# Kernel tuning notes

Measured on AMD Instinct MI355X. Metric: run time of the kernel, lower is better.

The kernel has to match this reference:

```python
import jax, jax.numpy as jnp
import numpy as np
from jax import lax

HEADS = 8
DIM_HEAD = 64
MODALITIES = 8
QUERY_DIM = 128
INNER = HEADS * DIM_HEAD  # 512


def _conv(x, w):
    # x: (b, Cin, H, W), w: (Cout, Cin, kh, kw), VALID padding (padding done manually)
    return lax.conv_general_dilated(x, w, window_strides=(1, 1), padding='VALID',
                                    dimension_numbers=('NCHW', 'OIHW', 'NCHW'))


def _reflect_pad_w(x):
    # ReflectionPad2d((2,2,0,0)): pad width (last) axis by 2 on each side
    return jnp.pad(x, ((0, 0), (0, 0), (0, 0), (2, 2)), mode='reflect')


def setup_inputs() -> dict:
    key = jax.random.key(0)
    k1, k2, k3, k4 = jax.random.split(key, 4)
    b, n, m, c = 2, 4096, MODALITIES, QUERY_DIM
    x = jax.random.normal(k1, (b, n, m, c), dtype=jnp.float32)
    Wq = jax.random.normal(k2, (INNER, c, 1, 5), dtype=jnp.float32) * 0.02
    Wkv = jax.random.normal(k3, (2 * INNER, c, 1, 5), dtype=jnp.float32) * 0.02
    Wout = jax.random.normal(k4, (c * m, INNER, m, 5), dtype=jnp.float32) * 0.02
    return {"x": x, "Wq": Wq, "Wkv": Wkv, "Wout": Wout}


def reference(x, Wq, Wkv, Wout):
    b, n, m, c = x.shape
    h, d = HEADS, DIM_HEAD
    scale = d ** -0.5

    xp = _reflect_pad_w(jnp.transpose(x, (0, 3, 2, 1)))  # (b, c, m, n+4)
    q = _conv(xp, Wq)                                     # (b, h*d, m, n)
    kv = _conv(xp, Wkv)                                   # (b, 2*h*d, m, n)
    k, v = kv[:, :h * d], kv[:, h * d:]

    # channel axis (h d) split: h outer, d inner -> (b, h, d, m, n)
    q = q.reshape(b, h, d, m, n)
    k = k.reshape(b, h, d, m, n)
    v = v.reshape(b, h, d, m, n)

    # attention over sequence axis n; feature dim is (m d) per head
    sim = jnp.einsum('bhdmi,bhdmj->bhij', q, k) * scale   # (b, h, n, n)
    attn = jax.nn.softmax(sim, axis=-1)
    out = jnp.einsum('bhij,bhdmj->bhdmi', attn, v)        # (b, h, d, m, n)

    out = out.reshape(b, h * d, m, n)                     # 'b (h d) m n'
    o = _conv(_reflect_pad_w(out), Wout)                  # (b, c*m, 1, n)
    o = o.reshape(b, c, m, 1, n)[:, :, :, 0, :]           # squeeze height-1 dim -> (b, c, m, n)
    return o.reshape(x.shape)                             # torch .view(x_shape) is a raw reshape
```

## Files before the change

### kernel.cpp

```cpp
#include <hip/hip_runtime.h>
#include <stdint.h>


typedef __attribute__((ext_vector_type(8))) short short8;
typedef __attribute__((ext_vector_type(4))) short short4v;
typedef __attribute__((ext_vector_type(2))) short short2v;
typedef __attribute__((ext_vector_type(4))) float f32x4;
typedef __attribute__((ext_vector_type(16))) float f32x16;

__device__ __forceinline__ f32x4 mfma16(short8 a, short8 b, f32x4 c) {
  return __builtin_amdgcn_mfma_f32_16x16x32_bf16(a, b, c, 0, 0, 0);
}
__device__ __forceinline__ f32x16 mfma32(short8 a, short8 b, f32x16 c) {
  return __builtin_amdgcn_mfma_f32_32x32x16_bf16(a, b, c, 0, 0, 0);
}

__device__ __forceinline__ unsigned short f2bf(float f) {
  union { float f; uint32_t u; } v; v.f = f;
  uint32_t r = (v.u + 0x7fffu + ((v.u >> 16) & 1u)) >> 16;
  return (unsigned short)r;
}

__device__ __forceinline__ uint32_t cvtpk(float lo, float hi) {
  uint32_t r;
  asm volatile("v_cvt_pk_bf16_f32 %0, %1, %2" : "=v"(r) : "v"(lo), "v"(hi));
  return r;
}
__device__ __forceinline__ void plswap(uint32_t& a, uint32_t& b) {
  asm volatile("v_permlane32_swap_b32 %0, %1" : "+v"(a), "+v"(b));
}

__device__ __forceinline__ int refl4096(int p) {
  p = p < 0 ? -p : p;
  return p >= 4096 ? 8190 - p : p;
}

__device__ __forceinline__ void gl_lds16(const void* g, void* l) {
  __builtin_amdgcn_global_load_lds(
      (const __attribute__((address_space(1))) void*)g,
      (__attribute__((address_space(3))) void*)l, 16, 0, 0);
}

__global__ void k_convw_qkv(const float* __restrict__ Wq,
                            const float* __restrict__ Wkv,
                            unsigned short* __restrict__ out) {
  int e = blockIdx.x * 256 + threadIdx.x;
  int oc = e / 640, k = e - oc * 640;
  int ci = k & 127, t = k >> 7;
  float w = (oc < 512) ? Wq[oc * 640 + ci * 5 + t]
                       : Wkv[(oc - 512) * 640 + ci * 5 + t];
  out[e] = f2bf(w);
}

__global__ __launch_bounds__(256)
void k_convw_out(const float* __restrict__ Wout,
                 unsigned short* __restrict__ out) {
  __shared__ unsigned short row_l[20480];
  const int oc = blockIdx.x;
  const int tid = threadIdx.x;
  const float* src = Wout + (size_t)oc * 20480;
#pragma unroll
  for (int i0 = 0; i0 < 5120; i0 += 256) {
    int i = i0 + tid;
    f32x4 v = *(const f32x4*)(src + (size_t)i * 4);
    short4v pk;
    pk[0] = (short)f2bf(v[0]); pk[1] = (short)f2bf(v[1]);
    pk[2] = (short)f2bf(v[2]); pk[3] = (short)f2bf(v[3]);
    *(short4v*)(row_l + i * 4) = pk;
  }
  __syncthreads();
  unsigned short* drow = out + (size_t)oc * 20480;
#pragma unroll
  for (int r0 = 0; r0 < 20480; r0 += 512) {
    int e = r0 + tid * 2;
    int t0 = e >> 12, ft0 = e & 4095;
    int t1 = (e + 1) >> 12, ft1 = (e + 1) & 4095;
    short2v pk;
    pk[0] = (short)row_l[(ft0 >> 3) * 40 + (ft0 & 7) * 5 + t0];
    pk[1] = (short)row_l[(ft1 >> 3) * 40 + (ft1 & 7) * 5 + t1];
    *(short2v*)(drow + e) = pk;
  }
}

__global__ __launch_bounds__(256, 2)
void k_qkv(const float* __restrict__ x, const unsigned short* __restrict__ Wb,
           unsigned short* __restrict__ Qg, unsigned short* __restrict__ Kg,
           unsigned short* __restrict__ Vg, int b) {
  __shared__ __align__(16) unsigned short As[128 * 64];
  __shared__ __align__(16) unsigned short Bs[128 * 64];
  const int tid = threadIdx.x;
  const int lane = tid & 63, w = tid >> 6;
  const int wr = w >> 1, wc = w & 1;
  const int l15 = lane & 15, lg = lane >> 4;
  const int p0 = blockIdx.x * 128;
  const int ocb = blockIdx.y * 128;
  const int m = blockIdx.z;

  f32x4 acc[4][4];
#pragma unroll
  for (int i = 0; i < 4; i++)
#pragma unroll
    for (int j = 0; j < 4; j++) acc[i][j] = (f32x4){0.f, 0.f, 0.f, 0.f};

  for (int ks = 0; ks < 10; ks++) {
    const int t = ks >> 1;
    const int ci0 = (ks & 1) << 6;
    __syncthreads();
#pragma unroll
    for (int rr = 0; rr < 8; rr++) {
      int slot = tid + (rr << 8);
      int row = slot >> 4, c4 = slot & 15;
      int xn = refl4096(p0 + row - 2 + t);
      const f32x4 v = *(const f32x4*)(x + ((size_t)b * 4096 + xn) * 1024 +
                                      m * 128 + ci0 + (c4 << 2));
      short4v pk;
      pk[0] = (short)f2bf(v[0]); pk[1] = (short)f2bf(v[1]);
      pk[2] = (short)f2bf(v[2]); pk[3] = (short)f2bf(v[3]);
      int byte = (row << 7) + ((((c4 >> 1) ^ (row & 7))) << 4) + ((c4 & 1) << 3);
      *(short4v*)((char*)As + byte) = pk;
    }
#pragma unroll
    for (int c = 0; c < 4; c++) {
      int sb = ((c << 2) + w) << 6;
      int slot = sb + lane;
      int row = slot >> 3, cc = slot & 7;
      int cs = cc ^ (row & 7);
      gl_lds16(Wb + (size_t)(ocb + row) * 640 + (ks << 6) + (cs << 3),
               (char*)Bs + (size_t)sb * 16);
    }
    __syncthreads();
#pragma unroll
    for (int kk = 0; kk < 2; kk++) {
      short8 af[4], bq[4];
#pragma unroll
      for (int i = 0; i < 4; i++) {
        int row = (wr << 6) + (i << 4) + l15;
        af[i] = *(const short8*)((char*)As + (row << 7) +
                                 ((((kk << 2) + lg) ^ (row & 7)) << 4));
      }
#pragma unroll
      for (int j = 0; j < 4; j++) {
        int row = (wc << 6) + (j << 4) + l15;
        bq[j] = *(const short8*)((char*)Bs + (row << 7) +
                                 ((((kk << 2) + lg) ^ (row & 7)) << 4));
      }
#pragma unroll
      for (int i = 0; i < 4; i++)
#pragma unroll
        for (int j = 0; j < 4; j++) acc[i][j] = mfma16(af[i], bq[j], acc[i][j]);
    }
  }

  const int region = ocb >> 9;
  const float QSCALE = 0.18033688f;
#pragma unroll
  for (int i = 0; i < 4; i++) {
    const int posb = p0 + (wr << 6) + (i << 4) + (lg << 2);
#pragma unroll
    for (int j = 0; j < 4; j++) {
      const int oc = ocb + (wc << 6) + (j << 4) + l15;
      const int ocr = oc & 511;
      const int hh = ocr >> 6, dd = ocr & 63;
      const int f = (dd << 3) + m;
      if (region == 0) {
        size_t base = (size_t)hh * 4096 * 512 + f;
#pragma unroll
        for (int r = 0; r < 4; r++)
          Qg[base + (size_t)(posb + r) * 512] = f2bf(acc[i][j][r] * QSCALE);
      } else if (region == 1) {
        size_t base = (size_t)hh * 4096 * 512 + f;
#pragma unroll
        for (int r = 0; r < 4; r++)
          Kg[base + (size_t)(posb + r) * 512] = f2bf(acc[i][j][r]);
      } else {
        short4v pk;
#pragma unroll
        for (int r = 0; r < 4; r++) pk[r] = (short)f2bf(acc[i][j][r]);
        *(short4v*)(Vg + ((size_t)hh * 512 + f) * 4096 + posb) = pk;
      }
    }
  }
}

__global__ __launch_bounds__(512, 2)
void k_attn(const unsigned short* __restrict__ Qg,
            const unsigned short* __restrict__ Kg,
            const unsigned short* __restrict__ Vg,
            unsigned short* __restrict__ AO) {
  __shared__ __align__(16) char lds[139776];
  char* Kt = lds;
  char* Vt0 = lds + 32768;
  char* Vt1 = lds + 65536;
  char* Sx = lds + 98304;
  float* Ls = (float*)(lds + 139264);

  const int tid = threadIdx.x;
  const int lane = tid & 63, w = tid >> 6;
  const int l31 = lane & 31, hi = lane >> 5;
  const int wpair = w >> 1, whalf = w & 1;
  const int h = blockIdx.y;
  const int qbase = blockIdx.x * 128 + wpair * 32;
  const int fh = whalf << 8;

  const size_t kb = (size_t)h * 4096 * 512;
  const size_t vb = (size_t)h * 512 * 4096;

  short8 q[16];
  {
    const unsigned short* qp =
        Qg + ((size_t)h * 4096 + qbase + l31) * 512 + fh + hi * 8;
#pragma unroll
    for (int ks = 0; ks < 16; ks++) q[ks] = *(const short8*)(qp + ks * 16);
  }

  f32x16 o[8];
#pragma unroll
  for (int t = 0; t < 8; t++)
#pragma unroll
    for (int e = 0; e < 16; e++) o[t][e] = 0.f;
  float lacc = 0.f;

  const int rb = l31 >> 1;
  const int swz = rb & 7;
  const int cg0 = ((l31 & 1) << 2) + hi;
  const int voff1 = rb * 128 + ((cg0 ^ swz) << 4);
  const int voff2 = rb * 128 + (((cg0 + 2) ^ swz) << 4);

  char* sxw = Sx + w * 5120 + lane * 80;
  char* sxp = Sx + (w ^ 1) * 5120 + lane * 80;

  union U { uint32_t d[4]; short8 s; };

  auto stageK = [&](int it) {
    const int key0 = it << 5;
#pragma unroll
    for (int i = 0; i < 4; i++) {
      int s = tid + (i << 9);
      int r = s >> 6, c = s & 63;
      gl_lds16(Kg + kb + (size_t)(key0 + r) * 512 + ((c ^ r) << 3),
               Kt + (size_t)s * 16);
    }
  };
  auto stageV = [&](int it, char* Vt) {
    const int key0 = it << 5;
#pragma unroll
    for (int i = 0; i < 4; i++) {
      int s = tid + (i << 9);
      int rp = s >> 3, c = s & 7;
      int cu = c ^ (rp & 7);
      int f = (rp << 1) + (cu >> 2);
      gl_lds16(Vg + vb + (size_t)f * 4096 + key0 + ((cu & 3) << 3),
               Vt + (size_t)s * 16);
    }
  };

  stageK(0);
  stageV(0, Vt0);

  for (int it = 0; it < 128; it++) {
    char* Vt = (it & 1) ? Vt1 : Vt0;
    char* Vn = (it & 1) ? Vt0 : Vt1;
    __syncthreads();

    f32x16 st;
#pragma unroll
    for (int e = 0; e < 16; e++) st[e] = 0.f;
#pragma unroll
    for (int ks = 0; ks < 16; ks++) {
      int ch = ((fh >> 3) + (ks << 1) + hi) ^ l31;
      short8 kfrag = *(const short8*)(Kt + (l31 << 10) + (ch << 4));
      st = mfma32(kfrag, q[ks], st);
    }
#pragma unroll
    for (int j = 0; j < 4; j++) {
      f32x4 pw = (f32x4){st[4 * j], st[4 * j + 1], st[4 * j + 2], st[4 * j + 3]};
      *(f32x4*)(sxw + j * 16) = pw;
    }
    __syncthreads();

    if (it < 127) {
      stageK(it + 1);
      stageV(it + 1, Vn);
    }

#pragma unroll
    for (int j = 0; j < 4; j++) {
      f32x4 pv = *(const f32x4*)(sxp + j * 16);
      st[4 * j] += pv[0]; st[4 * j + 1] += pv[1];
      st[4 * j + 2] += pv[2]; st[4 * j + 3] += pv[3];
    }

    float p[16];
#pragma unroll
    for (int r = 0; r < 16; r++) p[r] = __builtin_amdgcn_exp2f(st[r]);
    lacc += ((p[0] + p[1]) + (p[2] + p[3])) + ((p[4] + p[5]) + (p[6] + p[7])) +
            (((p[8] + p[9]) + (p[10] + p[11])) +
             ((p[12] + p[13]) + (p[14] + p[15])));

    uint32_t d0 = cvtpk(p[0], p[1]),  d1 = cvtpk(p[2], p[3]);
    uint32_t d2 = cvtpk(p[4], p[5]),  d3 = cvtpk(p[6], p[7]);
    uint32_t d4 = cvtpk(p[8], p[9]),  d5 = cvtpk(p[10], p[11]);
    uint32_t d6 = cvtpk(p[12], p[13]), d7 = cvtpk(p[14], p[15]);
    plswap(d0, d2); plswap(d1, d3);
    plswap(d4, d6); plswap(d5, d7);
    U u1; u1.d[0] = d0; u1.d[1] = d1; u1.d[2] = d2; u1.d[3] = d3;
    U u2; u2.d[0] = d4; u2.d[1] = d5; u2.d[2] = d6; u2.d[3] = d7;

#pragma unroll
    for (int tt = 0; tt < 8; tt++) {
      const char* vrow = Vt + (((whalf << 3) + tt) << 11);
      short8 v1 = *(const short8*)(vrow + voff1);
      short8 v2 = *(const short8*)(vrow + voff2);
      o[tt] = mfma32(u1.s, v1, o[tt]);
      o[tt] = mfma32(u2.s, v2, o[tt]);
    }
  }

  lacc += __shfl_xor(lacc, 32, 64);
  if (whalf == 0) Ls[(wpair << 5) + l31] = lacc;
  __syncthreads();

  float linv[16];
#pragma unroll
  for (int r = 0; r < 16; r++) {
    int qq = (r & 3) + ((r >> 2) << 3) + (hi << 2);
    linv[r] = 1.f / Ls[(wpair << 5) + qq];
  }
#pragma unroll
  for (int tt = 0; tt < 8; tt++) {
    size_t col = (size_t)h * 512 + (((whalf << 3) + tt) << 5) + l31;
#pragma unroll
    for (int r = 0; r < 16; r++) {
      int qq = qbase + (r & 3) + ((r >> 2) << 3) + (hi << 2);
      AO[(size_t)qq * 4096 + col] = f2bf(o[tt][r] * linv[r]);
    }
  }
}

__global__ __launch_bounds__(512, 2)
void k_outconv(const unsigned short* __restrict__ AO,
               const unsigned short* __restrict__ WB,
               float* __restrict__ outp, int b) {
  __shared__ __align__(16) char Lc[46720];
  const int tid = threadIdx.x;
  const int lane = tid & 63, w = tid >> 6;
  const int wr = w >> 1, wc = w & 1;
  const int l15 = lane & 15, lg = lane >> 4;
  const int i0 = blockIdx.x * 256;
  const int ocb = blockIdx.y * 64;

  f32x4 acc[4][2];
#pragma unroll
  for (int i = 0; i < 4; i++)
#pragma unroll
    for (int j = 0; j < 2; j++) acc[i][j] = (f32x4){0.f, 0.f, 0.f, 0.f};

  size_t soff[6];
  bool sact[6];
#pragma unroll
  for (int i = 0; i < 6; i++) {
    int s = tid + (i << 9);
    sact[i] = (s < 2900);
    int sc = sact[i] ? s : 0;
    size_t off;
    if (sc < 1300) {
      int r = sc / 5, c = sc - r * 5;
      int cr = c < 4 ? c : 3;
      off = (size_t)refl4096(i0 + r - 2) * 4096 + ((cr ^ (r & 3)) << 3);
    } else {
      int sB = sc - 1300;
      int row = sB / 5, c = sB - row * 5;
      int cr = c < 4 ? c : 3;
      int t = row >> 6, qoc = row & 63;
      off = 0x80000000u + (size_t)(ocb + qoc) * 20480 + t * 4096 +
            ((cr ^ (row & 3)) << 3);
    }
    soff[i] = off;
  }

  for (int step = 0; step < 128; step++) {
    const int f0 = step << 5;
    __syncthreads();
#pragma unroll
    for (int i = 0; i < 6; i++) {
      if (sact[i]) {
        int s = tid + (i << 9);
        size_t off = soff[i];
        const unsigned short* src =
            (off & 0x80000000u) ? (WB + (off & 0x7fffffffu) + f0)
                                : (AO + off + f0);
        gl_lds16(src, Lc + (size_t)s * 16);
      }
    }
    __syncthreads();
#pragma unroll
    for (int t = 0; t < 5; t++) {
      short8 af[4], bq[2];
#pragma unroll
      for (int i = 0; i < 4; i++) {
        int r = (wr << 6) + (i << 4) + l15 + t;
        af[i] = *(const short8*)(Lc + r * 80 + ((lg ^ (r & 3)) << 4));
      }
#pragma unroll
      for (int j = 0; j < 2; j++) {
        int rowb = (t << 6) + (wc << 5) + (j << 4) + l15;
        bq[j] = *(const short8*)(Lc + 20800 + rowb * 80 +
                                 ((lg ^ (rowb & 3)) << 4));
      }
#pragma unroll
      for (int i = 0; i < 4; i++)
#pragma unroll
        for (int j = 0; j < 2; j++) acc[i][j] = mfma16(af[i], bq[j], acc[i][j]);
    }
  }
#pragma unroll
  for (int i = 0; i < 4; i++)
#pragma unroll
    for (int j = 0; j < 2; j++) {
      int oc = ocb + (wc << 5) + (j << 4) + l15;
      int pos = i0 + (wr << 6) + (i << 4) + (lg << 2);
      *(f32x4*)(outp + ((size_t)b * 1024 + oc) * 4096 + pos) = acc[i][j];
    }
}

extern "C" void kernel_launch(void* const* d_in, const int* in_sizes, int n_in,
                              void* d_out, int out_size, void* d_ws,
                              size_t ws_size, hipStream_t stream) {
  const float* x = (const float*)d_in[0];
  const float* Wq = (const float*)d_in[1];
  const float* Wkv = (const float*)d_in[2];
  const float* Wout = (const float*)d_in[3];
  float* out = (float*)d_out;
  char* ws = (char*)d_ws;

  const size_t SEG = 33554432;
  unsigned short* Qg = (unsigned short*)ws;
  unsigned short* Kg = (unsigned short*)(ws + SEG);
  unsigned short* Vg = (unsigned short*)(ws + 2 * SEG);
  unsigned short* AO = (unsigned short*)(ws + 3 * SEG);
  unsigned short* WB1 = (unsigned short*)(ws + 4 * SEG);
  unsigned short* WB2 = (unsigned short*)ws;

  k_convw_qkv<<<3840, 256, 0, stream>>>(Wq, Wkv, WB1);
  for (int b = 0; b < 2; b++) {
    k_qkv<<<dim3(32, 12, 8), 256, 0, stream>>>(x, WB1, Qg, Kg, Vg, b);
    k_attn<<<dim3(32, 8), 512, 0, stream>>>(Qg, Kg, Vg, AO);
    k_convw_out<<<1024, 256, 0, stream>>>(Wout, WB2);
    k_outconv<<<dim3(16, 16), 512, 0, stream>>>(AO, WB2, out, b);
  }
}
```

Measured before the change: 1.568 ms.

## Pre-convert x to bf16, direct-to-LDS loads, double-buffer outconv, shrink attn LDS

Adds a kernel that converts each batch of x to bf16 into the AO workspace. The QKV GEMM then stages its A tile with global_load_lds directly, with no per-element conversion in the loop. The output conv now double-buffers the AO tile in LDS, prefetching the next step while computing, and reads weight fragments straight from global memory into registers instead of staging them. The attention kernel's partial-score exchange buffer is relaid out to a 16-byte stride, which shrinks LDS use. The costs are an extra pass over x, reuse of the AO buffer as scratch, and uncached global weight loads on the outconv critical path.

Result: slower. 1.784 ms (+13.8%).

```diff
diff --git a/kernel.cpp b/kernel.cpp
--- a/kernel.cpp
+++ b/kernel.cpp
@@ -53,6 +53,21 @@
 }
 
 __global__ __launch_bounds__(256)
+void k_convx(const float* __restrict__ x, unsigned short* __restrict__ xb,
+             int b) {
+  int e = (blockIdx.x * 256 + threadIdx.x) * 8;
+  const float* src = x + (size_t)b * 4194304 + e;
+  f32x4 v0 = *(const f32x4*)src;
+  f32x4 v1 = *(const f32x4*)(src + 4);
+  short8 pk;
+  pk[0] = (short)f2bf(v0[0]); pk[1] = (short)f2bf(v0[1]);
+  pk[2] = (short)f2bf(v0[2]); pk[3] = (short)f2bf(v0[3]);
+  pk[4] = (short)f2bf(v1[0]); pk[5] = (short)f2bf(v1[1]);
+  pk[6] = (short)f2bf(v1[2]); pk[7] = (short)f2bf(v1[3]);
+  *(short8*)(xb + e) = pk;
+}
+
+__global__ __launch_bounds__(256)
 void k_convw_out(const float* __restrict__ Wout,
                  unsigned short* __restrict__ out) {
   __shared__ unsigned short row_l[20480];
@@ -83,9 +98,10 @@
 }
 
 __global__ __launch_bounds__(256, 2)
-void k_qkv(const float* __restrict__ x, const unsigned short* __restrict__ Wb,
+void k_qkv(const unsigned short* __restrict__ xb,
+           const unsigned short* __restrict__ Wb,
            unsigned short* __restrict__ Qg, unsigned short* __restrict__ Kg,
-           unsigned short* __restrict__ Vg, int b) {
+           unsigned short* __restrict__ Vg) {
   __shared__ __align__(16) unsigned short As[128 * 64];
   __shared__ __align__(16) unsigned short Bs[128 * 64];
   const int tid = threadIdx.x;
@@ -107,17 +123,13 @@
     const int ci0 = (ks & 1) << 6;
     __syncthreads();
 #pragma unroll
-    for (int rr = 0; rr < 8; rr++) {
-      int slot = tid + (rr << 8);
-      int row = slot >> 4, c4 = slot & 15;
+    for (int i = 0; i < 4; i++) {
+      int s = tid + (i << 8);
+      int row = s >> 3, c = s & 7;
+      int cs = c ^ (row & 7);
       int xn = refl4096(p0 + row - 2 + t);
-      const f32x4 v = *(const f32x4*)(x + ((size_t)b * 4096 + xn) * 1024 +
-                                      m * 128 + ci0 + (c4 << 2));
-      short4v pk;
-      pk[0] = (short)f2bf(v[0]); pk[1] = (short)f2bf(v[1]);
-      pk[2] = (short)f2bf(v[2]); pk[3] = (short)f2bf(v[3]);
-      int byte = (row << 7) + ((((c4 >> 1) ^ (row & 7))) << 4) + ((c4 & 1) << 3);
-      *(short4v*)((char*)As + byte) = pk;
+      gl_lds16(xb + (((size_t)xn << 3) + m) * 128 + ci0 + (cs << 3),
+               (char*)As + (size_t)s * 16);
     }
 #pragma unroll
     for (int c = 0; c < 4; c++) {
@@ -187,12 +199,12 @@
             const unsigned short* __restrict__ Kg,
             const unsigned short* __restrict__ Vg,
             unsigned short* __restrict__ AO) {
-  __shared__ __align__(16) char lds[139776];
+  __shared__ __align__(16) char lds[131584];
   char* Kt = lds;
   char* Vt0 = lds + 32768;
   char* Vt1 = lds + 65536;
   char* Sx = lds + 98304;
-  float* Ls = (float*)(lds + 139264);
+  float* Ls = (float*)(lds + 131072);
 
   const int tid = threadIdx.x;
   const int lane = tid & 63, w = tid >> 6;
@@ -226,8 +238,8 @@
   const int voff1 = rb * 128 + ((cg0 ^ swz) << 4);
   const int voff2 = rb * 128 + (((cg0 + 2) ^ swz) << 4);
 
-  char* sxw = Sx + w * 5120 + lane * 80;
-  char* sxp = Sx + (w ^ 1) * 5120 + lane * 80;
+  char* sxw = Sx + (w << 10) + (lane << 4);
+  char* sxp = Sx + ((w ^ 1) << 10) + (lane << 4);
 
   union U { uint32_t d[4]; short8 s; };
 
@@ -274,7 +286,7 @@
 #pragma unroll
     for (int j = 0; j < 4; j++) {
       f32x4 pw = (f32x4){st[4 * j], st[4 * j + 1], st[4 * j + 2], st[4 * j + 3]};
-      *(f32x4*)(sxw + j * 16) = pw;
+      *(f32x4*)(sxw + (j << 13)) = pw;
     }
     __syncthreads();
 
@@ -285,7 +297,7 @@
 
 #pragma unroll
     for (int j = 0; j < 4; j++) {
-      f32x4 pv = *(const f32x4*)(sxp + j * 16);
+      f32x4 pv = *(const f32x4*)(sxp + (j << 13));
       st[4 * j] += pv[0]; st[4 * j + 1] += pv[1];
       st[4 * j + 2] += pv[2]; st[4 * j + 3] += pv[3];
     }
@@ -341,7 +353,7 @@
 void k_outconv(const unsigned short* __restrict__ AO,
                const unsigned short* __restrict__ WB,
                float* __restrict__ outp, int b) {
-  __shared__ __align__(16) char Lc[46720];
+  __shared__ __align__(16) char La[2][20800];
   const int tid = threadIdx.x;
   const int lane = tid & 63, w = tid >> 6;
   const int wr = w >> 1, wc = w & 1;
@@ -355,62 +367,65 @@
 #pragma unroll
     for (int j = 0; j < 2; j++) acc[i][j] = (f32x4){0.f, 0.f, 0.f, 0.f};
 
-  size_t soff[6];
-  bool sact[6];
-#pragma unroll
-  for (int i = 0; i < 6; i++) {
+  size_t aoff[3];
+  bool aact[3];
+#pragma unroll
+  for (int i = 0; i < 3; i++) {
     int s = tid + (i << 9);
-    sact[i] = (s < 2900);
-    int sc = sact[i] ? s : 0;
-    size_t off;
-    if (sc < 1300) {
-      int r = sc / 5, c = sc - r * 5;
-      int cr = c < 4 ? c : 3;
-      off = (size_t)refl4096(i0 + r - 2) * 4096 + ((cr ^ (r & 3)) << 3);
-    } else {
-      int sB = sc - 1300;
-      int row = sB / 5, c = sB - row * 5;
-      int cr = c < 4 ? c : 3;
-      int t = row >> 6, qoc = row & 63;
-      off = 0x80000000u + (size_t)(ocb + qoc) * 20480 + t * 4096 +
-            ((cr ^ (row & 3)) << 3);
-    }
-    soff[i] = off;
-  }
+    aact[i] = (s < 1300);
+    int sc = aact[i] ? s : 0;
+    int r = sc / 5, c = sc - r * 5;
+    int cr = c < 4 ? c : 3;
+    aoff[i] = (size_t)refl4096(i0 + r - 2) * 4096 + ((cr ^ (r & 3)) << 3);
+  }
+
+  uint32_t wboff[5][2];
+#pragma unroll
+  for (int t = 0; t < 5; t++)
+#pragma unroll
+    for (int j = 0; j < 2; j++)
+      wboff[t][j] = (uint32_t)(ocb + (wc << 5) + (j << 4) + l15) * 20480u +
+                    (uint32_t)t * 4096u + (uint32_t)(lg << 3);
+
+  auto stageA = [&](int step, int d) {
+    const int f0 = step << 5;
+#pragma unroll
+    for (int i = 0; i < 3; i++) {
+      if (aact[i]) {
+        int s = tid + (i << 9);
+        gl_lds16(AO + aoff[i] + f0, La[d] + (size_t)s * 16);
+      }
+    }
+  };
+
+  stageA(0, 0);
 
   for (int step = 0; step < 128; step++) {
+    const int d = step & 1;
     const int f0 = step << 5;
     __syncthreads();
-#pragma unroll
-    for (int i = 0; i < 6; i++) {
-      if (sact[i]) {
-        int s = tid + (i << 9);
-        size_t off = soff[i];
-        const unsigned short* src =
-            (off & 0x80000000u) ? (WB + (off & 0x7fffffffu) + f0)
-                                : (AO + off + f0);
-        gl_lds16(src, Lc + (size_t)s * 16);
-      }
-    }
-    __syncthreads();
+    if (step < 127) stageA(step + 1, d ^ 1);
+
+    short8 wf[5][2];
+#pragma unroll
+    for (int t = 0; t < 5; t++)
+#pragma unroll
+      for (int j = 0; j < 2; j++)
+        wf[t][j] = *(const short8*)(WB + wboff[t][j] + f0);
+
 #pragma unroll
     for (int t = 0; t < 5; t++) {
-      short8 af[4], bq[2];
+      short8 af[4];
 #pragma unroll
       for (int i = 0; i < 4; i++) {
         int r = (wr << 6) + (i << 4) + l15 + t;
-        af[i] = *(const short8*)(Lc + r * 80 + ((lg ^ (r & 3)) << 4));
+        af[i] = *(const short8*)(La[d] + r * 80 + ((lg ^ (r & 3)) << 4));
       }
 #pragma unroll
-      for (int j = 0; j < 2; j++) {
-        int rowb = (t << 6) + (wc << 5) + (j << 4) + l15;
-        bq[j] = *(const short8*)(Lc + 20800 + rowb * 80 +
-                                 ((lg ^ (rowb & 3)) << 4));
-      }
-#pragma unroll
       for (int i = 0; i < 4; i++)
 #pragma unroll
-        for (int j = 0; j < 2; j++) acc[i][j] = mfma16(af[i], bq[j], acc[i][j]);
+        for (int j = 0; j < 2; j++)
+          acc[i][j] = mfma16(af[i], wf[t][j], acc[i][j]);
     }
   }
 #pragma unroll
@@ -438,12 +453,14 @@
   unsigned short* Kg = (unsigned short*)(ws + SEG);
   unsigned short* Vg = (unsigned short*)(ws + 2 * SEG);
   unsigned short* AO = (unsigned short*)(ws + 3 * SEG);
+  unsigned short* xb = AO;
   unsigned short* WB1 = (unsigned short*)(ws + 4 * SEG);
   unsigned short* WB2 = (unsigned short*)ws;
 
   k_convw_qkv<<<3840, 256, 0, stream>>>(Wq, Wkv, WB1);
   for (int b = 0; b < 2; b++) {
-    k_qkv<<<dim3(32, 12, 8), 256, 0, stream>>>(x, WB1, Qg, Kg, Vg, b);
+    k_convx<<<2048, 256, 0, stream>>>(x, xb, b);
+    k_qkv<<<dim3(32, 12, 8), 256, 0, stream>>>(xb, WB1, Qg, Kg, Vg);
     k_attn<<<dim3(32, 8), 512, 0, stream>>>(Qg, Kg, Vg, AO);
     k_convw_out<<<1024, 256, 0, stream>>>(Wout, WB2);
     k_outconv<<<dim3(16, 16), 512, 0, stream>>>(AO, WB2, out, b);
```
